# Kernel tuning notes

Hardware: AMD Instinct MI355X
Metric: run time of the kernel (lower is better)

Reference implementation:

```python
import jax, jax.numpy as jnp
import numpy as np

N = 20000      # nodes
E = 320000     # edges (before self loops)
IN = 128       # in_channels
H = 8          # heads
C = 33         # hidden per head
D = H * C      # 264, concat width
OUT = D // 2   # 132, readout width
NEG_SLOPE = 0.2


def setup_inputs() -> dict:
    key = jax.random.key(0)
    ks = jax.random.split(key, 24)
    inp = {}
    inp["x"] = jax.random.normal(ks[0], (N, IN), jnp.float32)
    inp["edge_index"] = jax.random.randint(ks[1], (2, E), 0, N, dtype=jnp.int32)
    in_dims = [IN, D, D, D]
    k = 2
    for i, din in enumerate(in_dims):
        s = 1.0 / np.sqrt(din)
        inp[f"W{i}"] = jax.random.normal(ks[k], (din, D), jnp.float32) * s; k += 1
        inp[f"a_src{i}"] = jax.random.normal(ks[k], (H, C), jnp.float32) * 0.1; k += 1
        inp[f"a_dst{i}"] = jax.random.normal(ks[k], (H, C), jnp.float32) * 0.1; k += 1
        inp[f"b{i}"] = jnp.zeros((D,), jnp.float32)
    inp["W_head"] = jax.random.normal(ks[k], (D, OUT), jnp.float32) * (1.0 / np.sqrt(D)); k += 1
    inp["b_head"] = jnp.zeros((OUT,), jnp.float32)
    return inp


def _gat_layer(h, src, dst, W, a_s, a_d, b):
    # h: [N, din] -> out: [N, H*C]
    xh = (h @ W).reshape(-1, H, C)                  # [N, H, C]
    alpha_s = jnp.sum(xh * a_s, axis=-1)            # [N, H]
    alpha_d = jnp.sum(xh * a_d, axis=-1)            # [N, H]
    e = jax.nn.leaky_relu(alpha_s[src] + alpha_d[dst], NEG_SLOPE)  # [E', H]
    # segment softmax over incoming edges per destination node
    m = jax.ops.segment_max(e, dst, num_segments=N)                # [N, H]
    ex = jnp.exp(e - m[dst])
    denom = jax.ops.segment_sum(ex, dst, num_segments=N)           # [N, H]
    alpha = ex / (denom[dst] + 1e-16)                              # [E', H]
    msg = xh[src] * alpha[..., None]                               # [E', H, C]
    out = jax.ops.segment_sum(msg, dst, num_segments=N)            # [N, H, C]
    return out.reshape(-1, D) + b


def reference(x, edge_index, W0, a_src0, a_dst0, b0, W1, a_src1, a_dst1, b1,
              W2, a_src2, a_dst2, b2, W3, a_src3, a_dst3, b3, W_head, b_head):
    # PyG GATConv default add_self_loops=True
    loops = jnp.arange(N, dtype=edge_index.dtype)
    src = jnp.concatenate([edge_index[0], loops])
    dst = jnp.concatenate([edge_index[1], loops])
    params = [(W0, a_src0, a_dst0, b0), (W1, a_src1, a_dst1, b1),
              (W2, a_src2, a_dst2, b2), (W3, a_src3, a_dst3, b3)]
    h = x
    for (W, a_s, a_d, b) in params:
        h = _gat_layer(h, src, dst, W, a_s, a_d, b)
        h = jax.nn.elu(h)
    z = h @ W_head + b_head  # readout (dropout off at inference)
    return z
```

## Files before the change

kernel.cpp:

```cpp
#include <hip/hip_runtime.h>
#include <hip/hip_bf16.h>

#define N_NODES 20000
#define N_EDGES 320000
#define TOT_E   (N_EDGES + N_NODES)
#define IN_CH   128
#define HEADS   8
#define CH      33
#define DD      264
#define OUTW    132
#define NEG     0.2f

#define LDB     272
#define LDA     320
#define NT_HID  18
#define NT_HEAD 12
#define PK0     4
#define PKH     10
#define PKO     10

typedef unsigned short ushort;
typedef unsigned int uint32;
typedef short bf16x8 __attribute__((ext_vector_type(8)));
typedef float f32x4  __attribute__((ext_vector_type(4)));

__device__ inline void split2(float v, ushort& hi, ushort& lo) {
    __hip_bfloat16 h = __float2bfloat16(v);
    float r = v - __bfloat162float(h);
    __hip_bfloat16 l = __float2bfloat16(r);
    hi = *(ushort*)&h;
    lo = *(ushort*)&l;
}

__device__ inline float bf2f(ushort u) {
    union { unsigned int i; float f; } c;
    c.i = ((unsigned int)u) << 16;
    return c.f;
}

__device__ inline float bflo(uint32 d) {
    union { unsigned int i; float f; } c;
    c.i = d << 16;
    return c.f;
}
__device__ inline float bfhi(uint32 d) {
    union { unsigned int i; float f; } c;
    c.i = d & 0xffff0000u;
    return c.f;
}


__global__ void deg_k(const int* __restrict__ ei, int* __restrict__ deg) {
    int e = blockIdx.x * 256 + threadIdx.x;
    if (e >= TOT_E) return;
    int dst = (e < N_EDGES) ? ei[N_EDGES + e] : (e - N_EDGES);
    atomicAdd(&deg[dst], 1);
}

__global__ __launch_bounds__(1024) void scan_k(const int* __restrict__ deg,
                                               int* __restrict__ rowp) {
    __shared__ int part[1024];
    const int PER = 20;
    int t = threadIdx.x;
    int base = t * PER;
    int s = 0;
    for (int i = 0; i < PER; ++i) {
        int idx = base + i;
        if (idx < N_NODES) s += deg[idx];
    }
    part[t] = s;
    __syncthreads();
    for (int off = 1; off < 1024; off <<= 1) {
        int v = 0;
        if (t >= off) v = part[t - off];
        __syncthreads();
        part[t] += v;
        __syncthreads();
    }
    int run = part[t] - s;
    for (int i = 0; i < PER; ++i) {
        int idx = base + i;
        if (idx < N_NODES) { rowp[idx] = run; run += deg[idx]; }
    }
    if (t == 1023) rowp[N_NODES] = part[1023];
}

__global__ void fill_k(const int* __restrict__ ei, const int* __restrict__ rowp,
                       int* __restrict__ cur, int* __restrict__ csr) {
    int e = blockIdx.x * 256 + threadIdx.x;
    if (e >= TOT_E) return;
    int src, dst;
    if (e < N_EDGES) { src = ei[e]; dst = ei[N_EDGES + e]; }
    else             { src = dst = e - N_EDGES; }
    int p = atomicAdd(&cur[dst], 1);
    csr[rowp[dst] + p] = src;
}


__global__ void splitx_k(const float* __restrict__ x, ushort* __restrict__ ahi) {
    int idx = blockIdx.x * 256 + threadIdx.x;
    if (idx >= N_NODES * IN_CH) return;
    int n = idx >> 7, k = idx & 127;
    __hip_bfloat16 h = __float2bfloat16(x[idx]);
    ahi[(size_t)n * LDA + k] = *(ushort*)&h;
}


__device__ void convw_one(const float* W, const float* a_s, const float* a_d,
                          int K, int NC, int NT, ushort* fhi, ushort* flo, int gid) {
    int p = gid / (NT * 64);
    int rem = gid % (NT * 64);
    int t = rem >> 6, c = rem & 63;
    int kq = c >> 4, m = c & 15;
    int n = t * 16 + m;
    bool stats = (a_s != nullptr) && (t == NT - 1);
    ushort hi8[8], lo8[8];
#pragma unroll
    for (int j = 0; j < 8; ++j) {
        int k = p * 32 + kq * 8 + j;
        float v = 0.f;
        if (k < K) {
            if (stats) {
                const float* av = (m < 8) ? a_s : a_d;
                int h = (m < 8) ? m : m - 8;
                const float* wr = W + (size_t)k * NC + h * CH;
                float s = 0.f;
                for (int cc = 0; cc < CH; ++cc) s += wr[cc] * av[h * CH + cc];
                v = s;
            } else if (n < NC) {
                v = W[(size_t)k * NC + n];
            }
        }
        split2(v, hi8[j], lo8[j]);
    }
    size_t o = ((size_t)gid) * 8;
#pragma unroll
    for (int j = 0; j < 8; ++j) { fhi[o + j] = hi8[j]; flo[o + j] = lo8[j]; }
}

#define SEG0 (PK0 * NT_HID * 64)
#define SEGH (PKH * NT_HID * 64)
#define SEGO (PKO * NT_HEAD * 64)

__global__ void convall_k(
    const float* W0, const float* W1, const float* W2, const float* W3, const float* Wh,
    const float* as0, const float* as1, const float* as2, const float* as3,
    const float* ad0, const float* ad1, const float* ad2, const float* ad3,
    ushort* f0h, ushort* f0l, ushort* f1h, ushort* f1l, ushort* f2h, ushort* f2l,
    ushort* f3h, ushort* f3l, ushort* fhh, ushort* fhl) {
    int gid = blockIdx.x * 256 + threadIdx.x;
    if (gid < SEG0) { convw_one(W0, as0, ad0, IN_CH, DD, NT_HID, f0h, f0l, gid); return; }
    gid -= SEG0;
    if (gid < SEGH) { convw_one(W1, as1, ad1, DD, DD, NT_HID, f1h, f1l, gid); return; }
    gid -= SEGH;
    if (gid < SEGH) { convw_one(W2, as2, ad2, DD, DD, NT_HID, f2h, f2l, gid); return; }
    gid -= SEGH;
    if (gid < SEGH) { convw_one(W3, as3, ad3, DD, DD, NT_HID, f3h, f3l, gid); return; }
    gid -= SEGH;
    if (gid < SEGO) { convw_one(Wh, nullptr, nullptr, DD, OUTW, NT_HEAD, fhh, fhl, gid); }
}


template<bool USE3, int TG>
__global__ __launch_bounds__(256) void gemm4_k(
    const ushort* __restrict__ Ahi, const ushort* __restrict__ Alo, int kpairs,
    const ushort* __restrict__ Bhi, const ushort* __restrict__ Blo, int NTtot, int statsY,
    ushort* __restrict__ Cb16, float* __restrict__ as_, float* __restrict__ ad_,
    float* __restrict__ C, int ldc, int ncguard, const float* __restrict__ bias) {
    extern __shared__ ushort smem[];
    ushort* AlH = smem;
    ushort* BlH = smem + 8192;
    ushort* EXT = smem + 8192 + 2 * TG * 512;
    ushort* AlL = EXT;
    ushort* BlL = EXT + 8192;
    ushort* BstL = EXT;

    int tid = threadIdx.x;
    int m0 = blockIdx.x * 128;
    int t0 = blockIdx.y * TG;
    bool sg = ((int)blockIdx.y == statsY);

    f32x4 acc[2][TG];
#pragma unroll
    for (int mt = 0; mt < 2; ++mt)
#pragma unroll
        for (int t = 0; t < TG; ++t) acc[mt][t] = (f32x4){0.f, 0.f, 0.f, 0.f};

    int w = tid >> 6, lane = tid & 63;
    int csA = (lane ^ ((lane >> 4) << 1)) * 8;

    for (int pp = 0; pp < kpairs; ++pp) {
        int nA = USE3 ? 2048 : 1024;
        for (int id = tid; id < nA; id += 256) {
            int hl = id >> 10;
            int cid = id & 1023;
            int mrow = cid >> 3, kq8 = cid & 7;
            int panel = kq8 >> 2, kq = kq8 & 3;
            int gm = m0 + mrow;
            uint4 v = {0, 0, 0, 0};
            if (gm < N_NODES) {
                const ushort* src = (hl ? Alo : Ahi) + (size_t)gm * LDA + pp * 64 + kq8 * 8;
                v = *(const uint4*)src;
            }
            int c = kq * 16 + (mrow & 15);
            int cs = c ^ ((c >> 4) << 1);
            ushort* dst = (hl ? AlL : AlH) + panel * 4096 + (mrow >> 4) * 512 + cs * 8;
            *(uint4*)dst = v;
        }
        for (int id = tid; id < 2 * TG * 64; id += 256) {
            int c = id & 63;
            int r = id >> 6;
            int t = r % TG;
            int panel = r / TG;
            const ushort* src = Bhi + ((size_t)((pp * 2 + panel) * NTtot + t0 + t) * 64 + c) * 8;
            *(uint4*)&BlH[(panel * TG + t) * 512 + c * 8] = *(const uint4*)src;
        }
        if (USE3) {
            for (int id = tid; id < 2 * TG * 64; id += 256) {
                int c = id & 63;
                int r = id >> 6;
                int t = r % TG;
                int panel = r / TG;
                const ushort* src = Blo + ((size_t)((pp * 2 + panel) * NTtot + t0 + t) * 64 + c) * 8;
                *(uint4*)&BlL[(panel * TG + t) * 512 + c * 8] = *(const uint4*)src;
            }
        } else if (sg) {
            for (int id = tid; id < 2 * 64; id += 256) {
                int c = id & 63;
                int panel = id >> 6;
                const ushort* src = Blo + ((size_t)((pp * 2 + panel) * NTtot + t0 + TG - 1) * 64 + c) * 8;
                *(uint4*)&BstL[panel * 512 + c * 8] = *(const uint4*)src;
            }
        }
        __syncthreads();

#pragma unroll
        for (int panel = 0; panel < 2; ++panel) {
            bf16x8 a0 = *(const bf16x8*)&AlH[panel * 4096 + (2 * w) * 512 + csA];
            bf16x8 a1 = *(const bf16x8*)&AlH[panel * 4096 + (2 * w + 1) * 512 + csA];
            bf16x8 l0, l1;
            if (USE3) {
                l0 = *(const bf16x8*)&AlL[panel * 4096 + (2 * w) * 512 + csA];
                l1 = *(const bf16x8*)&AlL[panel * 4096 + (2 * w + 1) * 512 + csA];
            }
#pragma unroll
            for (int t = 0; t < TG; ++t) {
                bf16x8 bh = *(const bf16x8*)&BlH[(panel * TG + t) * 512 + lane * 8];
                acc[0][t] = __builtin_amdgcn_mfma_f32_16x16x32_bf16(a0, bh, acc[0][t], 0, 0, 0);
                acc[1][t] = __builtin_amdgcn_mfma_f32_16x16x32_bf16(a1, bh, acc[1][t], 0, 0, 0);
                if (USE3) {
                    bf16x8 bl = *(const bf16x8*)&BlL[(panel * TG + t) * 512 + lane * 8];
                    acc[0][t] = __builtin_amdgcn_mfma_f32_16x16x32_bf16(a0, bl, acc[0][t], 0, 0, 0);
                    acc[1][t] = __builtin_amdgcn_mfma_f32_16x16x32_bf16(a1, bl, acc[1][t], 0, 0, 0);
                    acc[0][t] = __builtin_amdgcn_mfma_f32_16x16x32_bf16(l0, bh, acc[0][t], 0, 0, 0);
                    acc[1][t] = __builtin_amdgcn_mfma_f32_16x16x32_bf16(l1, bh, acc[1][t], 0, 0, 0);
                } else if (t == TG - 1 && sg) {
                    bf16x8 bst = *(const bf16x8*)&BstL[panel * 512 + lane * 8];
                    acc[0][t] = __builtin_amdgcn_mfma_f32_16x16x32_bf16(a0, bst, acc[0][t], 0, 0, 0);
                    acc[1][t] = __builtin_amdgcn_mfma_f32_16x16x32_bf16(a1, bst, acc[1][t], 0, 0, 0);
                }
            }
        }
        __syncthreads();
    }

    int col = lane & 15;
#pragma unroll
    for (int mt = 0; mt < 2; ++mt) {
        int rbase = m0 + (2 * w + mt) * 16 + ((lane >> 4) << 2);
#pragma unroll
        for (int t = 0; t < TG; ++t) {
            int tg = t0 + t;
#pragma unroll
            for (int r = 0; r < 4; ++r) {
                int gm = rbase + r;
                if (gm >= N_NODES) continue;
                float v = acc[mt][t][r];
                if (C) {
                    int gn = tg * 16 + col;
                    if (gn < ncguard) C[(size_t)gm * ldc + gn] = v + bias[gn];
                } else if (tg < 17) {
                    __hip_bfloat16 bv = __float2bfloat16(v);
                    Cb16[(size_t)gm * LDB + tg * 16 + col] = *(ushort*)&bv;
                } else {
                    if (col < 8) as_[(size_t)gm * 8 + col] = v;
                    else         ad_[(size_t)gm * 8 + col - 8] = v;
                }
            }
        }
    }
}


__global__ __launch_bounds__(64) void gat_k(
    const ushort* __restrict__ xb, const float* __restrict__ as_,
    const float* __restrict__ ad_, const int* __restrict__ rowp,
    const int* __restrict__ csr, const float* __restrict__ bias,
    ushort* __restrict__ outhi, ushort* __restrict__ outlo) {
    int lane = threadIdx.x;
    int node = blockIdx.x;
    int r0 = rowp[node], dg = rowp[node + 1] - r0;

    __shared__ float lex[64][9];
    __shared__ int   lsrc[64];

    float ad[8];
#pragma unroll
    for (int h = 0; h < 8; ++h) ad[h] = ad_[node * 8 + h];

    int ha = (4 * lane) / 33;
    int hb = (4 * lane + 3) / 33;
    bool m1 = ((4 * lane + 1) / 33) != ha;
    bool m2 = ((4 * lane + 2) / 33) != ha;

    float4 a0 = {0.f, 0.f, 0.f, 0.f}, a1 = {0.f, 0.f, 0.f, 0.f};
    float sm[8] = {0.f, 0.f, 0.f, 0.f, 0.f, 0.f, 0.f, 0.f};

    int nchunks = (dg + 63) >> 6;
    for (int c = 0; c < nchunks; ++c) {
        int base = c << 6, j = base + lane;
        int s = node;
        float p8[8];
#pragma unroll
        for (int h = 0; h < 8; ++h) p8[h] = 0.f;
        if (j < dg) {
            s = csr[r0 + j];
            const float* ap = as_ + (size_t)s * 8;
#pragma unroll
            for (int h = 0; h < 8; ++h) {
                float e = ap[h] + ad[h];
                e = e > 0.f ? e : NEG * e;
                float p = __expf(e);
                p8[h] = p;
                sm[h] += p;
            }
        }
        lsrc[lane] = s * LDB;
#pragma unroll
        for (int h = 0; h < 8; ++h) lex[lane][h] = p8[h];
        __builtin_amdgcn_wave_barrier();

        int rem = dg - base;
        int cnt = rem > 64 ? 64 : rem;
        int cnt4 = (cnt + 3) & ~3;
        for (int jj = 0; jj < cnt4; jj += 4) {
            int o0 = lsrc[jj + 0], o1 = lsrc[jj + 1];
            int o2 = lsrc[jj + 2], o3 = lsrc[jj + 3];
            const uint2* p0 = (const uint2*)(xb + (size_t)(unsigned)o0);
            const uint2* p1 = (const uint2*)(xb + (size_t)(unsigned)o1);
            const uint2* p2 = (const uint2*)(xb + (size_t)(unsigned)o2);
            const uint2* p3 = (const uint2*)(xb + (size_t)(unsigned)o3);
            uint2 v0 = p0[lane], v1 = p1[lane], v2 = p2[lane], v3 = p3[lane];
            uint2 t0 = p0[64 + (lane & 1)], t1 = p1[64 + (lane & 1)];
            uint2 t2 = p2[64 + (lane & 1)], t3 = p3[64 + (lane & 1)];
#pragma unroll
            for (int e = 0; e < 4; ++e) {
                const float* xr = lex[jj + e];
                float xa = xr[ha], xbv = xr[hb], x7 = xr[7];
                float x1 = m1 ? xbv : xa;
                float x2 = m2 ? xbv : xa;
                uint2 v = (e == 0) ? v0 : (e == 1) ? v1 : (e == 2) ? v2 : v3;
                uint2 t = (e == 0) ? t0 : (e == 1) ? t1 : (e == 2) ? t2 : t3;
                a0.x += xa  * bflo(v.x);
                a0.y += x1  * bfhi(v.x);
                a0.z += x2  * bflo(v.y);
                a0.w += xbv * bfhi(v.y);
                a1.x += x7 * bflo(t.x);
                a1.y += x7 * bfhi(t.x);
                a1.z += x7 * bflo(t.y);
                a1.w += x7 * bfhi(t.y);
            }
        }
        __builtin_amdgcn_wave_barrier();
    }

    float iv[8];
#pragma unroll
    for (int h = 0; h < 8; ++h) {
        float s = sm[h];
        for (int off = 32; off; off >>= 1) s += __shfl_xor(s, off, 64);
        iv[h] = 1.0f / (s + 1e-16f);
    }

#pragma unroll
    for (int k = 0; k < 2; ++k) {
        int i4 = lane + 64 * k;
        if (i4 < 66) {
            float4 a = (k == 0) ? a0 : a1;
            float vals[4] = {a.x, a.y, a.z, a.w};
            int hds[4];
            if (k == 0) {
                hds[0] = ha; hds[1] = m1 ? hb : ha; hds[2] = m2 ? hb : ha; hds[3] = hb;
            } else {
                hds[0] = hds[1] = hds[2] = hds[3] = 7;
            }
            float4 bb = *(const float4*)(bias + i4 * 4);
            float bv4[4] = {bb.x, bb.y, bb.z, bb.w};
            ushort hi4[4], lo4[4];
#pragma unroll
            for (int j = 0; j < 4; ++j) {
                float v = vals[j] * iv[hds[j]] + bv4[j];
                v = v > 0.f ? v : (__expf(v) - 1.f);
                split2(v, hi4[j], lo4[j]);
            }
            size_t o = (size_t)node * LDA + i4 * 4;
            *(ushort4*)(outhi + o) = *(ushort4*)hi4;
            if (outlo) *(ushort4*)(outlo + o) = *(ushort4*)lo4;
        } else if (i4 < 80) {
            ushort4 z = {0, 0, 0, 0};
            size_t o = (size_t)node * LDA + i4 * 4;
            *(ushort4*)(outhi + o) = z;
            if (outlo) *(ushort4*)(outlo + o) = z;
        }
    }
}


extern "C" void kernel_launch(void* const* d_in, const int* in_sizes, int n_in,
                              void* d_out, int out_size, void* d_ws, size_t ws_size,
                              hipStream_t stream) {
    const float* x  = (const float*)d_in[0];
    const int*   ei = (const int*)d_in[1];
    const float* W[4]  = {(const float*)d_in[2],  (const float*)d_in[6],
                          (const float*)d_in[10], (const float*)d_in[14]};
    const float* As[4] = {(const float*)d_in[3],  (const float*)d_in[7],
                          (const float*)d_in[11], (const float*)d_in[15]};
    const float* Ad[4] = {(const float*)d_in[4],  (const float*)d_in[8],
                          (const float*)d_in[12], (const float*)d_in[16]};
    const float* Bb[4] = {(const float*)d_in[5],  (const float*)d_in[9],
                          (const float*)d_in[13], (const float*)d_in[17]};
    const float* Wh = (const float*)d_in[18];
    const float* bh = (const float*)d_in[19];

    char* p = (char*)d_ws;
    ushort* hBb  = (ushort*)p;          p += (size_t)N_NODES * LDB * 2;
    ushort* hAhi = (ushort*)p;          p += (size_t)N_NODES * LDA * 2;
    ushort* hAlo = (ushort*)p;          p += (size_t)N_NODES * LDA * 2;
    float* as_  = (float*)p;            p += (size_t)N_NODES * HEADS * 4;
    float* ad_  = (float*)p;            p += (size_t)N_NODES * HEADS * 4;
    const int wsz0 = PK0 * NT_HID * 512;
    const int wszH = PKH * NT_HID * 512;
    const int wszO = PKO * NT_HEAD * 512;
    ushort* wfhi[4]; ushort* wflo[4];
    for (int l = 0; l < 4; ++l) {
        int sz = (l == 0) ? wsz0 : wszH;
        wfhi[l] = (ushort*)p; p += (size_t)sz * 2;
        wflo[l] = (ushort*)p; p += (size_t)sz * 2;
    }
    ushort* whhi = (ushort*)p; p += (size_t)wszO * 2;
    ushort* whlo = (ushort*)p; p += (size_t)wszO * 2;
    int* deg  = (int*)p;  p += N_NODES * 4;
    int* cur  = (int*)p;  p += N_NODES * 4;
    int* rowp = (int*)p;  p += (N_NODES + 1) * 4;
    int* csr  = (int*)p;  p += (size_t)TOT_E * 4;

    hipMemsetAsync(deg, 0, sizeof(int) * 2 * N_NODES, stream);
    int egrid = (TOT_E + 255) / 256;
    deg_k<<<egrid, 256, 0, stream>>>(ei, deg);
    scan_k<<<1, 1024, 0, stream>>>(deg, rowp);
    fill_k<<<egrid, 256, 0, stream>>>(ei, rowp, cur, csr);

    splitx_k<<<(N_NODES * IN_CH + 255) / 256, 256, 0, stream>>>(x, hAhi);
    {
        int tot = SEG0 + 3 * SEGH + SEGO;
        convall_k<<<(tot + 255) / 256, 256, 0, stream>>>(
            W[0], W[1], W[2], W[3], Wh,
            As[0], As[1], As[2], As[3],
            Ad[0], Ad[1], Ad[2], Ad[3],
            wfhi[0], wflo[0], wfhi[1], wflo[1], wfhi[2], wflo[2],
            wfhi[3], wflo[3], whhi, whlo);
    }

    dim3 gG((N_NODES + 127) / 128, NT_HID / 6);
    dim3 gO((N_NODES + 127) / 128, NT_HEAD / 6);
    size_t smHid = (size_t)(8192 + 2 * 6 * 512 + 2 * 512) * 2;
    size_t smHead = (size_t)(8192 + 2 * 6 * 512 + 8192 + 2 * 6 * 512) * 2;

    for (int l = 0; l < 4; ++l) {
        int kpairs = (l == 0) ? PK0 / 2 : PKH / 2;
        gemm4_k<false, 6><<<gG, 256, smHid, stream>>>(hAhi, nullptr, kpairs,
                                                      wfhi[l], wflo[l], NT_HID, 2,
                                                      hBb, as_, ad_, nullptr, 0, 0, nullptr);
        gat_k<<<N_NODES, 64, 0, stream>>>(hBb, as_, ad_, rowp, csr, Bb[l],
                                          hAhi, (l == 3) ? hAlo : nullptr);
    }

    gemm4_k<true, 6><<<gO, 256, smHead, stream>>>(hAhi, hAlo, PKO / 2,
                                                  whhi, whlo, NT_HEAD, -1,
                                                  nullptr, nullptr, nullptr,
                                                  (float*)d_out, OUTW, OUTW, bh);
}
```

Baseline: 423.1 us.

## Process two nodes per wavefront in GAT aggregation with 16-byte gathers

The aggregation kernel now splits each 64-lane wave into two 32-lane halves, each handling its own destination node. Each lane covers 8 channels using 16-byte loads instead of 8-byte loads, and the edge chunk size drops to 32. The aim is to halve the block count, raise bytes per gather instruction, and reduce lanes idling on low-degree nodes. The cost is divergence when the two nodes in a wave have different degrees, since both halves loop to the larger chunk count, plus more registers per lane.

```diff
diff --git a/kernel.cpp b/kernel.cpp
--- a/kernel.cpp
+++ b/kernel.cpp
@@ -298,27 +298,36 @@
     const int* __restrict__ csr, const float* __restrict__ bias,
     ushort* __restrict__ outhi, ushort* __restrict__ outlo) {
     int lane = threadIdx.x;
-    int node = blockIdx.x;
+    int half = lane >> 5, l32 = lane & 31;
+    int node = blockIdx.x * 2 + half;
     int r0 = rowp[node], dg = rowp[node + 1] - r0;
 
-    __shared__ float lex[64][9];
-    __shared__ int   lsrc[64];
+    __shared__ float lex[2][32][9];
+    __shared__ int   lsrc[2][32];
 
     float ad[8];
 #pragma unroll
     for (int h = 0; h < 8; ++h) ad[h] = ad_[node * 8 + h];
 
-    int ha = (4 * lane) / 33;
-    int hb = (4 * lane + 3) / 33;
-    bool m1 = ((4 * lane + 1) / 33) != ha;
-    bool m2 = ((4 * lane + 2) / 33) != ha;
-
-    float4 a0 = {0.f, 0.f, 0.f, 0.f}, a1 = {0.f, 0.f, 0.f, 0.f};
+    int cb = l32 * 8;
+    int ha = cb / 33;
+    int hb = (cb + 7) / 33;
+    bool mm[8];
+#pragma unroll
+    for (int j = 0; j < 8; ++j) mm[j] = ((cb + j) / 33) != ha;
+
+    float a0[8];
+#pragma unroll
+    for (int j = 0; j < 8; ++j) a0[j] = 0.f;
+    float a1[4] = {0.f, 0.f, 0.f, 0.f};
     float sm[8] = {0.f, 0.f, 0.f, 0.f, 0.f, 0.f, 0.f, 0.f};
 
-    int nchunks = (dg + 63) >> 6;
-    for (int c = 0; c < nchunks; ++c) {
-        int base = c << 6, j = base + lane;
+    int mych = (dg + 31) >> 5;
+    int och = __shfl_xor(mych, 32, 64);
+    int maxch = mych > och ? mych : och;
+
+    for (int c = 0; c < maxch; ++c) {
+        int base = c << 5, j = base + l32;
         int s = node;
         float p8[8];
 #pragma unroll
@@ -335,40 +344,46 @@
                 sm[h] += p;
             }
         }
-        lsrc[lane] = s * LDB;
-#pragma unroll
-        for (int h = 0; h < 8; ++h) lex[lane][h] = p8[h];
+        lsrc[half][l32] = s * LDB;
+#pragma unroll
+        for (int h = 0; h < 8; ++h) lex[half][l32][h] = p8[h];
         __builtin_amdgcn_wave_barrier();
 
         int rem = dg - base;
-        int cnt = rem > 64 ? 64 : rem;
+        int cnt = rem < 0 ? 0 : (rem > 32 ? 32 : rem);
         int cnt4 = (cnt + 3) & ~3;
         for (int jj = 0; jj < cnt4; jj += 4) {
-            int o0 = lsrc[jj + 0], o1 = lsrc[jj + 1];
-            int o2 = lsrc[jj + 2], o3 = lsrc[jj + 3];
-            const uint2* p0 = (const uint2*)(xb + (size_t)(unsigned)o0);
-            const uint2* p1 = (const uint2*)(xb + (size_t)(unsigned)o1);
-            const uint2* p2 = (const uint2*)(xb + (size_t)(unsigned)o2);
-            const uint2* p3 = (const uint2*)(xb + (size_t)(unsigned)o3);
-            uint2 v0 = p0[lane], v1 = p1[lane], v2 = p2[lane], v3 = p3[lane];
-            uint2 t0 = p0[64 + (lane & 1)], t1 = p1[64 + (lane & 1)];
-            uint2 t2 = p2[64 + (lane & 1)], t3 = p3[64 + (lane & 1)];
+            int o0 = lsrc[half][jj + 0], o1 = lsrc[half][jj + 1];
+            int o2 = lsrc[half][jj + 2], o3 = lsrc[half][jj + 3];
+            const uint4* p0 = (const uint4*)(xb + (size_t)(unsigned)o0);
+            const uint4* p1 = (const uint4*)(xb + (size_t)(unsigned)o1);
+            const uint4* p2 = (const uint4*)(xb + (size_t)(unsigned)o2);
+            const uint4* p3 = (const uint4*)(xb + (size_t)(unsigned)o3);
+            uint4 v0 = p0[l32], v1 = p1[l32], v2 = p2[l32], v3 = p3[l32];
+            const uint2* q0 = (const uint2*)p0;
+            const uint2* q1 = (const uint2*)p1;
+            const uint2* q2 = (const uint2*)p2;
+            const uint2* q3 = (const uint2*)p3;
+            uint2 t0 = q0[64 + (l32 & 1)], t1 = q1[64 + (l32 & 1)];
+            uint2 t2 = q2[64 + (l32 & 1)], t3 = q3[64 + (l32 & 1)];
 #pragma unroll
             for (int e = 0; e < 4; ++e) {
-                const float* xr = lex[jj + e];
+                const float* xr = lex[half][jj + e];
                 float xa = xr[ha], xbv = xr[hb], x7 = xr[7];
-                float x1 = m1 ? xbv : xa;
-                float x2 = m2 ? xbv : xa;
-                uint2 v = (e == 0) ? v0 : (e == 1) ? v1 : (e == 2) ? v2 : v3;
+                uint4 v = (e == 0) ? v0 : (e == 1) ? v1 : (e == 2) ? v2 : v3;
                 uint2 t = (e == 0) ? t0 : (e == 1) ? t1 : (e == 2) ? t2 : t3;
-                a0.x += xa  * bflo(v.x);
-                a0.y += x1  * bfhi(v.x);
-                a0.z += x2  * bflo(v.y);
-                a0.w += xbv * bfhi(v.y);
-                a1.x += x7 * bflo(t.x);
-                a1.y += x7 * bfhi(t.x);
-                a1.z += x7 * bflo(t.y);
-                a1.w += x7 * bfhi(t.y);
+                a0[0] += (mm[0] ? xbv : xa) * bflo(v.x);
+                a0[1] += (mm[1] ? xbv : xa) * bfhi(v.x);
+                a0[2] += (mm[2] ? xbv : xa) * bflo(v.y);
+                a0[3] += (mm[3] ? xbv : xa) * bfhi(v.y);
+                a0[4] += (mm[4] ? xbv : xa) * bflo(v.z);
+                a0[5] += (mm[5] ? xbv : xa) * bfhi(v.z);
+                a0[6] += (mm[6] ? xbv : xa) * bflo(v.w);
+                a0[7] += (mm[7] ? xbv : xa) * bfhi(v.w);
+                a1[0] += x7 * bflo(t.x);
+                a1[1] += x7 * bfhi(t.x);
+                a1[2] += x7 * bflo(t.y);
+                a1[3] += x7 * bfhi(t.y);
             }
         }
         __builtin_amdgcn_wave_barrier();
@@ -378,39 +393,51 @@
 #pragma unroll
     for (int h = 0; h < 8; ++h) {
         float s = sm[h];
-        for (int off = 32; off; off >>= 1) s += __shfl_xor(s, off, 64);
+        for (int off = 16; off; off >>= 1) s += __shfl_xor(s, off, 64);
         iv[h] = 1.0f / (s + 1e-16f);
     }
 
-#pragma unroll
-    for (int k = 0; k < 2; ++k) {
-        int i4 = lane + 64 * k;
-        if (i4 < 66) {
-            float4 a = (k == 0) ? a0 : a1;
-            float vals[4] = {a.x, a.y, a.z, a.w};
-            int hds[4];
-            if (k == 0) {
-                hds[0] = ha; hds[1] = m1 ? hb : ha; hds[2] = m2 ? hb : ha; hds[3] = hb;
-            } else {
-                hds[0] = hds[1] = hds[2] = hds[3] = 7;
-            }
-            float4 bb = *(const float4*)(bias + i4 * 4);
-            float bv4[4] = {bb.x, bb.y, bb.z, bb.w};
-            ushort hi4[4], lo4[4];
-#pragma unroll
-            for (int j = 0; j < 4; ++j) {
-                float v = vals[j] * iv[hds[j]] + bv4[j];
-                v = v > 0.f ? v : (__expf(v) - 1.f);
-                split2(v, hi4[j], lo4[j]);
-            }
-            size_t o = (size_t)node * LDA + i4 * 4;
-            *(ushort4*)(outhi + o) = *(ushort4*)hi4;
-            if (outlo) *(ushort4*)(outlo + o) = *(ushort4*)lo4;
-        } else if (i4 < 80) {
-            ushort4 z = {0, 0, 0, 0};
-            size_t o = (size_t)node * LDA + i4 * 4;
-            *(ushort4*)(outhi + o) = z;
-            if (outlo) *(ushort4*)(outlo + o) = z;
+    {
+        float iva = iv[ha], ivb = iv[hb];
+        ushort hi8[8], lo8[8];
+        float4 b0 = *(const float4*)(bias + cb);
+        float4 b1 = *(const float4*)(bias + cb + 4);
+        float bv4[8] = {b0.x, b0.y, b0.z, b0.w, b1.x, b1.y, b1.z, b1.w};
+#pragma unroll
+        for (int j = 0; j < 8; ++j) {
+            float v = a0[j] * (mm[j] ? ivb : iva) + bv4[j];
+            v = v > 0.f ? v : (__expf(v) - 1.f);
+            split2(v, hi8[j], lo8[j]);
+        }
+        size_t o = (size_t)node * LDA + cb;
+        *(ushort4*)(outhi + o) = *(ushort4*)&hi8[0];
+        *(ushort4*)(outhi + o + 4) = *(ushort4*)&hi8[4];
+        if (outlo) {
+            *(ushort4*)(outlo + o) = *(ushort4*)&lo8[0];
+            *(ushort4*)(outlo + o + 4) = *(ushort4*)&lo8[4];
+        }
+    }
+    if (l32 < 2) {
+        ushort hi4[4], lo4[4];
+        float4 bt = *(const float4*)(bias + 256 + l32 * 4);
+        float bv4[4] = {bt.x, bt.y, bt.z, bt.w};
+#pragma unroll
+        for (int j = 0; j < 4; ++j) {
+            float v = a1[j] * iv[7] + bv4[j];
+            v = v > 0.f ? v : (__expf(v) - 1.f);
+            split2(v, hi4[j], lo4[j]);
+        }
+        size_t o = (size_t)node * LDA + 256 + l32 * 4;
+        *(ushort4*)(outhi + o) = *(ushort4*)hi4;
+        if (outlo) *(ushort4*)(outlo + o) = *(ushort4*)lo4;
+    } else if (l32 < 9) {
+        ushort4 z = {0, 0, 0, 0};
+        size_t o = (size_t)node * LDA + 264 + (l32 - 2) * 8;
+        *(ushort4*)(outhi + o) = z;
+        *(ushort4*)(outhi + o + 4) = z;
+        if (outlo) {
+            *(ushort4*)(outlo + o) = z;
+            *(ushort4*)(outlo + o + 4) = z;
         }
     }
 }
@@ -481,8 +508,8 @@
         gemm4_k<false, 6><<<gG, 256, smHid, stream>>>(hAhi, nullptr, kpairs,
                                                       wfhi[l], wflo[l], NT_HID, 2,
                                                       hBb, as_, ad_, nullptr, 0, 0, nullptr);
-        gat_k<<<N_NODES, 64, 0, stream>>>(hBb, as_, ad_, rowp, csr, Bb[l],
-                                          hAhi, (l == 3) ? hAlo : nullptr);
+        gat_k<<<N_NODES / 2, 64, 0, stream>>>(hBb, as_, ad_, rowp, csr, Bb[l],
+                                              hAhi, (l == 3) ? hAlo : nullptr);
     }
 
     gemm4_k<true, 6><<<gO, 256, smHead, stream>>>(hAhi, hAlo, PKO / 2,
```

New measurement: 417.1 us. Within noise of the previous version (-1.4%).
